# Optimization experiments

Measured on AMD Instinct MI355X. Metric: run time of the kernel, lower is better.

The kernel has to match this reference:

```python
import jax, jax.numpy as jnp
import numpy as np

CS = 5           # context_size
PAD = CS // 2    # spatial padding
EPS = 1e-12      # torch F.normalize eps


def setup_inputs() -> dict:
    key = jax.random.key(0)
    k1, k2, k3 = jax.random.split(key, 3)
    B, C, H, W = 8, 1024, 64, 64
    OC, INC = 1024, C + CS * CS  # 1049 input channels to 1x1 conv
    feature = jax.random.normal(k1, (B, C, H, W), dtype=jnp.float32)
    conv_w = jax.random.normal(k2, (OC, INC), dtype=jnp.float32) * 0.02
    conv_b = jax.random.normal(k3, (OC,), dtype=jnp.float32) * 0.02
    return {"feature": feature, "conv_w": conv_w, "conv_b": conv_b}


def reference(feature, conv_w, conv_b):
    b, c, h, w = feature.shape
    # L2-normalize over channel dim (torch normalize: x / max(||x||, eps))
    norm = jnp.sqrt(jnp.sum(feature * feature, axis=1, keepdims=True))
    fn = feature / jnp.maximum(norm, EPS)
    fp = jnp.pad(fn, ((0, 0), (0, 0), (PAD, PAD), (PAD, PAD)))
    # Windowed cosine-similarity cost volume: 25 fixed shifts (small static loop)
    sims = []
    for cc in range(CS):      # column shift (outer, matches torch ordering)
        for r in range(CS):   # row shift
            sims.append(jnp.sum(fp[:, :, r:h + r, cc:w + cc] * fn, axis=1))
    vol = jnp.stack(sims, axis=1)              # [b, 25, h, w]
    x = jnp.concatenate([feature, vol], axis=1)  # [b, c+25, h, w]
    # 1x1 conv == per-pixel GEMM over channels
    out = jnp.einsum('bihw,oi->bohw', x, conv_w) + conv_b[None, :, None, None]
    return jax.nn.relu(out)
```

## Files before the change

kernel.cpp:

```cpp
#include <hip/hip_runtime.h>
#include <stdint.h>

#define C_DIM 1024
#define HW    4096
#define KPAD  1056
#define KIN   1049
#define NPIX  32768
#define NCHUNK 16

typedef __bf16 bf16x8 __attribute__((ext_vector_type(8)));
typedef float  f32x4  __attribute__((ext_vector_type(4)));
typedef float  f32x2  __attribute__((ext_vector_type(2)));
typedef unsigned short u16x8 __attribute__((ext_vector_type(8)));

typedef const __attribute__((address_space(1))) void* gas_t;
typedef __attribute__((address_space(3))) void* las_t;

__device__ __forceinline__ unsigned short f2bf(float f) {
  unsigned u = __float_as_uint(f);
  unsigned r = u + 0x7FFFu + ((u >> 16) & 1u);
  return (unsigned short)(r >> 16);
}

__global__ __launch_bounds__(256) void prep_w(const float* __restrict__ cw,
                                              unsigned short* __restrict__ wb) {
  int o = blockIdx.x;
  for (int k = threadIdx.x; k < KPAD; k += 256) {
    float v = (k < KIN) ? cw[(size_t)o * KIN + k] : 0.0f;
    wb[(size_t)o * KPAD + k] = f2bf(v);
  }
}

__global__ __launch_bounds__(256) void pack_norm(const float* __restrict__ feat,
                                                 unsigned short* __restrict__ xb,
                                                 float* __restrict__ inv_norm,
                                                 int p_base) {
  __shared__ float tile[64][65];
  __shared__ float red[4][64];
  int t   = threadIdx.x;
  int p0l = blockIdx.x * 64;
  int p0g = p_base + p0l;
  int b   = p0g >> 12;
  int hw0 = p0g & 4095;
  int pl = t & 63;
  int q  = t >> 6;
  const float* fb = feat + (size_t)b * C_DIM * HW + hw0;
  float sumsq = 0.0f;
  for (int cc = 0; cc < 16; ++cc) {
#pragma unroll
    for (int i = 0; i < 16; ++i) {
      int cl = q + 4 * i;
      float v = fb[(size_t)(cc * 64 + cl) * HW + pl];
      sumsq += v * v;
      tile[cl][pl] = v;
    }
    __syncthreads();
#pragma unroll
    for (int r = 0; r < 2; ++r) {
      int id = t + r * 256;
      int pr = id >> 3;
      int c8 = id & 7;
      u16x8 hv;
#pragma unroll
      for (int e = 0; e < 8; ++e) hv[e] = f2bf(tile[c8 * 8 + e][pr]);
      size_t row = (size_t)(p0l + pr) * KPAD + cc * 64 + c8 * 8;
      *reinterpret_cast<u16x8*>(xb + row) = hv;
    }
    __syncthreads();
  }
  red[q][pl] = sumsq;
  __syncthreads();
  if (t < 64) {
    float s = red[0][t] + red[1][t] + red[2][t] + red[3][t];
    inv_norm[p0g + t] = 1.0f / fmaxf(sqrtf(s), 1e-12f);
  }
}

__global__ __launch_bounds__(256) void corr_part(const float* __restrict__ feat,
                                                 float* __restrict__ part) {
  __shared__ float lbuf[2][2][1288];
  int t = threadIdx.x;
  int bid = blockIdx.x;
  int chunk = bid & 15;
  int strip = (bid >> 4) & 3;
  int b     = bid >> 6;
  int h0 = strip * 16;
  int hr = t >> 4;
  int w0 = (t & 15) * 4;
  int wid = t >> 6;
  int lane = t & 63;

  const float* fb = feat + (size_t)b * C_DIM * HW;
  int rA = t >> 4;
  int cA = (t & 15) * 4;
  int hA = min(max(h0 - 2 + rA, 0), 63);
  int rB = 16 + wid;
  int cB = lane;
  int hB = min(max(h0 - 2 + rB, 0), 63);
  const float* srcA = fb + hA * 64 + cA;
  const float* srcB = fb + hB * 64 + cB;
  int c0 = chunk * 64;

  float acc[4][25];
#pragma unroll
  for (int j = 0; j < 4; ++j)
#pragma unroll
    for (int k = 0; k < 25; ++k) acc[j][k] = 0.0f;

  auto stage = [&](int bsel, int csel, int c) {
    float* dst = &lbuf[bsel][csel][4];
    size_t coff = (size_t)(c0 + c) * HW;
    __builtin_amdgcn_global_load_lds((gas_t)(srcA + coff),
                                     (las_t)(dst + wid * 256), 16, 0, 0);
    __builtin_amdgcn_global_load_lds((gas_t)(srcB + coff),
                                     (las_t)(dst + 1024 + wid * 64), 4, 0, 0);
  };

  stage(0, 0, 0);
  stage(0, 1, 1);
  __syncthreads();

  int cur = 0;
  for (int it = 0; it < 32; ++it) {
    if (it < 31) {
      stage(cur ^ 1, 0, 2 * it + 2);
      stage(cur ^ 1, 1, 2 * it + 3);
    }
#pragma unroll
    for (int cc = 0; cc < 2; ++cc) {
      const float* tile = &lbuf[cur][cc][4];
      const float* rp2 = tile + (hr + 2) * 64 + w0;
      f32x4 ctr4 = *reinterpret_cast<const f32x4*>(rp2);
#pragma unroll
      for (int r5 = 0; r5 < 5; ++r5) {
        const float* rp = tile + (hr + r5) * 64 + w0;
        f32x2 eL = *reinterpret_cast<const f32x2*>(rp - 2);
        f32x4 cc4 = *reinterpret_cast<const f32x4*>(rp);
        f32x2 eR = *reinterpret_cast<const f32x2*>(rp + 4);
        float win[8] = {eL[0], eL[1], cc4[0], cc4[1], cc4[2], cc4[3], eR[0], eR[1]};
#pragma unroll
        for (int j = 0; j < 4; ++j)
#pragma unroll
          for (int dcv = 0; dcv < 5; ++dcv)
            acc[j][dcv * 5 + r5] += win[j + dcv] * ctr4[j];
      }
    }
    __syncthreads();
    cur ^= 1;
  }

  int p0 = b * 4096 + (h0 + hr) * 64 + w0;
#pragma unroll
  for (int jj = 0; jj < 25; ++jj) {
    f32x4 v = {acc[0][jj], acc[1][jj], acc[2][jj], acc[3][jj]};
    *reinterpret_cast<f32x4*>(&part[(size_t)(chunk * 25 + jj) * NPIX + p0]) = v;
  }
}

__global__ __launch_bounds__(256) void corr_reduce(const float* __restrict__ part,
                                                   const float* __restrict__ inv_norm,
                                                   unsigned short* __restrict__ xb) {
  int pl = blockIdx.x * 256 + threadIdx.x;
  int w = pl & 63, h = (pl >> 6) & 63, b = pl >> 12;
  float inv_c = inv_norm[pl];
  float vals[32];
#pragma unroll
  for (int j = 0; j < 32; ++j) {
    float v = 0.0f;
    if (j < 25) {
      int dc = j / 5 - 2, dr = j % 5 - 2;
      int hh = h + dr, ww = w + dc;
      if (hh >= 0 && hh < 64 && ww >= 0 && ww < 64) {
        float s = 0.0f;
#pragma unroll
        for (int c = 0; c < NCHUNK; ++c)
          s += part[(size_t)(c * 25 + j) * NPIX + pl];
        v = s * inv_c * inv_norm[(b << 12) + (hh << 6) + ww];
      }
    }
    vals[j] = v;
  }
  unsigned short* xp = xb + (size_t)pl * KPAD + 1024;
#pragma unroll
  for (int g = 0; g < 4; ++g) {
    u16x8 pk;
#pragma unroll
    for (int e = 0; e < 8; ++e) pk[e] = f2bf(vals[g * 8 + e]);
    *reinterpret_cast<u16x8*>(xp + g * 8) = pk;
  }
}

__device__ __forceinline__ void stage_tile(const unsigned short* __restrict__ g,
                                           unsigned short* s, int t) {
#pragma unroll
  for (int r = 0; r < 2; ++r) {
    int idx = t + r * 256;
    int row = idx >> 2;
    int q = (idx & 3) ^ ((row >> 1) & 3);
    const unsigned short* gp = g + (size_t)row * KPAD + q * 8;
    unsigned short* sp = s + (t >> 6) * 512 + r * 2048;
    __builtin_amdgcn_global_load_lds((gas_t)gp, (las_t)sp, 16, 0, 0);
  }
}

__global__ __launch_bounds__(256, 2) void gemm_kernel(
    const unsigned short* __restrict__ xb, const unsigned short* __restrict__ wb,
    const float* __restrict__ bias, float* __restrict__ out,
    int p_base, int np) {
  __shared__ __align__(16) unsigned short sA[2][4096];
  __shared__ __align__(16) unsigned short sB[2][4096];
  int t = threadIdx.x;
  int lane = t & 63;
  int wid = t >> 6;
  int wm = wid >> 1, wn = wid & 1;
  int l15 = lane & 15, l4 = lane >> 4;
  int bid = blockIdx.x;
  int xcd = bid & 7;
  int j = bid >> 3;
  int o0 = (j & 7) * 128;
  int panel = xcd * (np >> 3) + (j >> 3);
  int p0l = panel * 128;

  f32x4 acc[4][4];
#pragma unroll
  for (int m = 0; m < 4; ++m)
#pragma unroll
    for (int n = 0; n < 4; ++n)
#pragma unroll
      for (int i = 0; i < 4; ++i) acc[m][n][i] = 0.0f;

  const unsigned short* A = wb + (size_t)o0 * KPAD;
  const unsigned short* B = xb + (size_t)p0l * KPAD;

  stage_tile(A, sA[0], t);
  stage_tile(B, sB[0], t);
  __syncthreads();

  int cur = 0;
  const int NKT = KPAD / 32;
  for (int kt = 0; kt < NKT; ++kt) {
    if (kt + 1 < NKT) {
      stage_tile(A + (kt + 1) * 32, sA[cur ^ 1], t);
      stage_tile(B + (kt + 1) * 32, sB[cur ^ 1], t);
    }
    bf16x8 bf[4];
#pragma unroll
    for (int n = 0; n < 4; ++n) {
      int rr = wn * 64 + n * 16 + l15;
      int off = rr * 32 + ((l4 ^ ((rr >> 1) & 3)) * 8);
      bf[n] = *reinterpret_cast<const bf16x8*>(&sB[cur][off]);
    }
#pragma unroll
    for (int m = 0; m < 4; ++m) {
      int ra = wm * 64 + m * 16 + l15;
      int off = ra * 32 + ((l4 ^ ((ra >> 1) & 3)) * 8);
      bf16x8 af = *reinterpret_cast<const bf16x8*>(&sA[cur][off]);
#pragma unroll
      for (int n = 0; n < 4; ++n)
        acc[m][n] = __builtin_amdgcn_mfma_f32_16x16x32_bf16(af, bf[n], acc[m][n], 0, 0, 0);
    }
    __syncthreads();
    cur ^= 1;
  }

#pragma unroll
  for (int m = 0; m < 4; ++m) {
    int ob = o0 + wm * 64 + m * 16 + l4 * 4;
    float b0 = bias[ob], b1 = bias[ob + 1], b2 = bias[ob + 2], b3 = bias[ob + 3];
#pragma unroll
    for (int n = 0; n < 4; ++n) {
      int pg = p_base + p0l + wn * 64 + n * 16 + l15;
      int bb = pg >> 12, hw = pg & 4095;
      float* op = out + ((size_t)bb << 22) + hw;
      op[(size_t)(ob + 0) << 12] = fmaxf(acc[m][n][0] + b0, 0.0f);
      op[(size_t)(ob + 1) << 12] = fmaxf(acc[m][n][1] + b1, 0.0f);
      op[(size_t)(ob + 2) << 12] = fmaxf(acc[m][n][2] + b2, 0.0f);
      op[(size_t)(ob + 3) << 12] = fmaxf(acc[m][n][3] + b3, 0.0f);
    }
  }
}

extern "C" void kernel_launch(void* const* d_in, const int* in_sizes, int n_in,
                              void* d_out, int out_size, void* d_ws, size_t ws_size,
                              hipStream_t stream) {
  const float* feat = (const float*)d_in[0];
  const float* cw   = (const float*)d_in[1];
  const float* cb   = (const float*)d_in[2];
  float* out = (float*)d_out;

  char* ws = (char*)d_ws;
  size_t SZ_X = (size_t)NPIX * KPAD * 2;
  size_t SZ_W = (size_t)1024 * KPAD * 2;
  unsigned short* xb = (unsigned short*)(ws);
  unsigned short* wb = (unsigned short*)(ws + SZ_X);
  float* inv_norm    = (float*)(ws + SZ_X + SZ_W);
  float* part        = (float*)(ws + SZ_X + SZ_W + (size_t)NPIX * 4);

  prep_w<<<1024, 256, 0, stream>>>(cw, wb);
  pack_norm<<<512, 256, 0, stream>>>(feat, xb, inv_norm, 0);
  corr_part<<<512, 256, 0, stream>>>(feat, part);
  corr_reduce<<<128, 256, 0, stream>>>(part, inv_norm, xb);
  gemm_kernel<<<2048, 256, 0, stream>>>(xb, wb, cb, out, 0, 256);
}
```

Measured before the change: 412.8 us.

## Triple-buffer LDS staging with partial vmcnt waits in corr and GEMM

Both the correlation partial kernel and the bf16 GEMM kernel move from a double-buffered LDS pipeline to a triple-buffered one, prefetching two stages ahead. Full __syncthreads waits are replaced with explicit s_waitcnt vmcnt(4) plus s_barrier, so one stage of global-to-LDS loads can stay in flight across the barrier. The goal is to hide global memory latency behind compute. The cost is more LDS per block, which may lower occupancy, and correctness now depends on the hand-counted vmcnt values matching the loads each thread issues.

Result: slower. 423.6 us (+2.6%).

```diff
diff --git a/kernel.cpp b/kernel.cpp
--- a/kernel.cpp
+++ b/kernel.cpp
@@ -78,7 +78,7 @@
 
 __global__ __launch_bounds__(256) void corr_part(const float* __restrict__ feat,
                                                  float* __restrict__ part) {
-  __shared__ float lbuf[2][2][1288];
+  __shared__ float lbuf[3][2][1288];
   int t = threadIdx.x;
   int bid = blockIdx.x;
   int chunk = bid & 15;
@@ -107,28 +107,29 @@
 #pragma unroll
     for (int k = 0; k < 25; ++k) acc[j][k] = 0.0f;
 
-  auto stage = [&](int bsel, int csel, int c) {
-    float* dst = &lbuf[bsel][csel][4];
-    size_t coff = (size_t)(c0 + c) * HW;
-    __builtin_amdgcn_global_load_lds((gas_t)(srcA + coff),
-                                     (las_t)(dst + wid * 256), 16, 0, 0);
-    __builtin_amdgcn_global_load_lds((gas_t)(srcB + coff),
-                                     (las_t)(dst + 1024 + wid * 64), 4, 0, 0);
+  auto stage2 = [&](int bsel, int c) {
+#pragma unroll
+    for (int cs = 0; cs < 2; ++cs) {
+      float* dst = &lbuf[bsel][cs][4];
+      size_t coff = (size_t)(c0 + c + cs) * HW;
+      __builtin_amdgcn_global_load_lds((gas_t)(srcA + coff),
+                                       (las_t)(dst + wid * 256), 16, 0, 0);
+      __builtin_amdgcn_global_load_lds((gas_t)(srcB + coff),
+                                       (las_t)(dst + 1024 + wid * 64), 4, 0, 0);
+    }
   };
 
-  stage(0, 0, 0);
-  stage(0, 1, 1);
-  __syncthreads();
-
-  int cur = 0;
+  stage2(0, 0);
+  stage2(1, 2);
+  asm volatile("s_waitcnt vmcnt(4)" ::: "memory");
+  __builtin_amdgcn_sched_barrier(0);
+  __builtin_amdgcn_s_barrier();
+
   for (int it = 0; it < 32; ++it) {
-    if (it < 31) {
-      stage(cur ^ 1, 0, 2 * it + 2);
-      stage(cur ^ 1, 1, 2 * it + 3);
-    }
+    if (it + 2 < 32) stage2((it + 2) % 3, 2 * (it + 2));
 #pragma unroll
     for (int cc = 0; cc < 2; ++cc) {
-      const float* tile = &lbuf[cur][cc][4];
+      const float* tile = &lbuf[it % 3][cc][4];
       const float* rp2 = tile + (hr + 2) * 64 + w0;
       f32x4 ctr4 = *reinterpret_cast<const f32x4*>(rp2);
 #pragma unroll
@@ -145,8 +146,10 @@
             acc[j][dcv * 5 + r5] += win[j + dcv] * ctr4[j];
       }
     }
-    __syncthreads();
-    cur ^= 1;
+    if (it < 30) asm volatile("s_waitcnt vmcnt(4)" ::: "memory");
+    else         asm volatile("s_waitcnt vmcnt(0)" ::: "memory");
+    __builtin_amdgcn_sched_barrier(0);
+    __builtin_amdgcn_s_barrier();
   }
 
   int p0 = b * 4096 + (h0 + hr) * 64 + w0;
@@ -207,8 +210,8 @@
     const unsigned short* __restrict__ xb, const unsigned short* __restrict__ wb,
     const float* __restrict__ bias, float* __restrict__ out,
     int p_base, int np) {
-  __shared__ __align__(16) unsigned short sA[2][4096];
-  __shared__ __align__(16) unsigned short sB[2][4096];
+  __shared__ __align__(16) unsigned short sA[3][4096];
+  __shared__ __align__(16) unsigned short sB[3][4096];
   int t = threadIdx.x;
   int lane = t & 63;
   int wid = t >> 6;
@@ -232,35 +235,42 @@
   const unsigned short* A = wb + (size_t)o0 * KPAD;
   const unsigned short* B = xb + (size_t)p0l * KPAD;
 
+  const int NKT = KPAD / 32;
   stage_tile(A, sA[0], t);
   stage_tile(B, sB[0], t);
-  __syncthreads();
-
-  int cur = 0;
-  const int NKT = KPAD / 32;
+  stage_tile(A + 32, sA[1], t);
+  stage_tile(B + 32, sB[1], t);
+  asm volatile("s_waitcnt vmcnt(4)" ::: "memory");
+  __builtin_amdgcn_sched_barrier(0);
+  __builtin_amdgcn_s_barrier();
+
   for (int kt = 0; kt < NKT; ++kt) {
-    if (kt + 1 < NKT) {
-      stage_tile(A + (kt + 1) * 32, sA[cur ^ 1], t);
-      stage_tile(B + (kt + 1) * 32, sB[cur ^ 1], t);
-    }
+    if (kt + 2 < NKT) {
+      stage_tile(A + (kt + 2) * 32, sA[(kt + 2) % 3], t);
+      stage_tile(B + (kt + 2) * 32, sB[(kt + 2) % 3], t);
+    }
+    const unsigned short* cA = sA[kt % 3];
+    const unsigned short* cB = sB[kt % 3];
     bf16x8 bf[4];
 #pragma unroll
     for (int n = 0; n < 4; ++n) {
       int rr = wn * 64 + n * 16 + l15;
       int off = rr * 32 + ((l4 ^ ((rr >> 1) & 3)) * 8);
-      bf[n] = *reinterpret_cast<const bf16x8*>(&sB[cur][off]);
+      bf[n] = *reinterpret_cast<const bf16x8*>(&cB[off]);
     }
 #pragma unroll
     for (int m = 0; m < 4; ++m) {
       int ra = wm * 64 + m * 16 + l15;
       int off = ra * 32 + ((l4 ^ ((ra >> 1) & 3)) * 8);
-      bf16x8 af = *reinterpret_cast<const bf16x8*>(&sA[cur][off]);
+      bf16x8 af = *reinterpret_cast<const bf16x8*>(&cA[off]);
 #pragma unroll
       for (int n = 0; n < 4; ++n)
         acc[m][n] = __builtin_amdgcn_mfma_f32_16x16x32_bf16(af, bf[n], acc[m][n], 0, 0, 0);
     }
-    __syncthreads();
-    cur ^= 1;
+    if (kt < NKT - 2) asm volatile("s_waitcnt vmcnt(4)" ::: "memory");
+    else              asm volatile("s_waitcnt vmcnt(0)" ::: "memory");
+    __builtin_amdgcn_sched_barrier(0);
+    __builtin_amdgcn_s_barrier();
   }
 
 #pragma unroll
```
